# Kernel tuning notes

Measured on AMD Instinct MI355X. Metric: run time of the kernel, lower is better.

The kernel has to match this reference:

```python
import jax, jax.numpy as jnp
import numpy as np

WIN = (9, 9, 9)
EPS = 1e-05


def setup_inputs() -> dict:
    key = jax.random.key(0)
    k1, k2 = jax.random.split(key)
    shape = (2, 1, 160, 160, 160)  # [B, C=1, D, H, W]
    x = jax.random.normal(k1, shape, dtype=jnp.float32)
    y = jax.random.normal(k2, shape, dtype=jnp.float32)
    return {"x": x, "y": y}


def _convn(z, kernel):
    # dense 3D box-sum conv, VALID (inputs are pre-padded), NCDHW layout
    return jax.lax.conv_general_dilated(
        z, kernel, window_strides=(1, 1, 1), padding='VALID',
        dimension_numbers=('NCDHW', 'OIDHW', 'NCDHW'))


def reference(x, y):
    p = tuple(w // 2 for w in WIN)  # (4, 4, 4)
    pad_cfg = ((0, 0), (0, 0), (p[0], p[0]), (p[1], p[1]), (p[2], p[2]))
    kernel = jnp.ones((1, 1) + WIN, dtype=x.dtype)

    x_pad = jnp.pad(x, pad_cfg, mode='edge')      # replicate padding
    y_pad = jnp.pad(y, pad_cfg, mode='edge')
    ones_pad = jnp.pad(jnp.ones_like(x), pad_cfg, mode='edge')

    N = _convn(ones_pad, kernel)                  # local window counts (all = 729 here)
    xm = _convn(x_pad, kernel) / N                # local mean of x
    ym = _convn(y_pad, kernel) / N                # local mean of y
    x2 = _convn(x_pad * x_pad, kernel) / N        # local E[x^2]
    y2 = _convn(y_pad * y_pad, kernel) / N        # local E[y^2]
    xy = _convn(x_pad * y_pad, kernel) / N        # local E[xy]

    cross = xy - xm * ym
    var_x = x2 - xm * xm
    var_y = y2 - ym * ym
    ncc = cross * cross / (var_x * var_y + EPS)
    return -jnp.mean(ncc)
```

## Files before the change

### kernel.cpp

```cpp
#include <hip/hip_runtime.h>

#define DIM 160
#define SLICE (DIM * DIM)
#define TH 16
#define TW 16
#define CD 40

#define HIDX(c,i,j) ((c)*680 + (i)*28 + (j))
#define UIDX(c,i,j) ((c)*260 + (i)*16 + (j))

#define WSLIDE(dst, V0,V1,V2,V3,V4,V5,V6,V7,V8,V9,V10,V11) do {            \
    float s_ = (V0)+(V1)+(V2)+(V3)+(V4)+(V5)+(V6)+(V7)+(V8);               \
    float4 o_; o_.x = s_;                                                  \
    s_ += (V9)  - (V0); o_.y = s_;                                         \
    s_ += (V10) - (V1); o_.z = s_;                                         \
    s_ += (V11) - (V2); o_.w = s_;                                         \
    (dst) = o_; } while (0)

static __device__ __forceinline__ void barrier_novm()
{
    asm volatile("s_waitcnt lgkmcnt(0)" ::: "memory");
    __builtin_amdgcn_s_barrier();
    asm volatile("" ::: "memory");
}

__global__ __launch_bounds__(256, 2)
void lncc_kernel(const float* __restrict__ x, const float* __restrict__ y,
                 float* __restrict__ out)
{
    __shared__ __align__(16) float H[5 * 680];
    __shared__ __align__(16) float U[5 * 260];
    __shared__ float wsum[4];

    const int t  = threadIdx.x;
    const int w0 = blockIdx.x * TW;
    const int h0 = blockIdx.y * TH;
    const int bz = blockIdx.z;
    const int b   = bz >> 2;
    const int zo0 = (bz & 3) * CD;

    const float* xb = x + (size_t)b * (DIM * SLICE);
    const float* yb = y + (size_t)b * (DIM * SLICE);

    const int lt  = t - 160;
    const int lrw = lt >> 2;
    const int lq  = lt & 3;
    const int ghr = min(max(h0 - 4 + lrw, 0), DIM - 1);
    const int rowoff = ghr * DIM;
    const int gws = w0 + 4 * lq - 4;
    const bool ok0 = (gws >= 0);
    const bool ok2 = (gws + 8 <= DIM - 4);
    const int jj = 4 * lq;

    const int hcc = t >> 3;
    const int hq  = (t >> 1) & 3;
    const int hh  = t & 1;
    const int hr0 = hh * 8;
    const int hjj = 4 * hq;

    const int i4 = t >> 4;
    const int j4 = t & 15;

    float hist[9][5];
    float rs[5] = {0.f, 0.f, 0.f, 0.f, 0.f};
    float acc = 0.f;

    float4 lx0, lx1, lx2, ly0, ly1, ly2;

    auto issue_loads = [&](int zsl) {
        const float* xs = xb + (size_t)zsl * SLICE + rowoff;
        const float* ys = yb + (size_t)zsl * SLICE + rowoff;
        lx1 = *reinterpret_cast<const float4*>(xs + gws + 4);
        ly1 = *reinterpret_cast<const float4*>(ys + gws + 4);
        if (ok0) {
            lx0 = *reinterpret_cast<const float4*>(xs + gws);
            ly0 = *reinterpret_cast<const float4*>(ys + gws);
        } else {
            const float v = xs[0];       lx0 = make_float4(v, v, v, v);
            const float w = ys[0];       ly0 = make_float4(w, w, w, w);
        }
        if (ok2) {
            lx2 = *reinterpret_cast<const float4*>(xs + gws + 8);
            ly2 = *reinterpret_cast<const float4*>(ys + gws + 8);
        } else {
            const float v = xs[DIM - 1]; lx2 = make_float4(v, v, v, v);
            const float w = ys[DIM - 1]; ly2 = make_float4(w, w, w, w);
        }
    };

    const int zfirst = zo0 - 4;
    if (t >= 160) issue_loads(max(zfirst, 0));

    for (int base = 0; base < 54; base += 9) {
        #pragma unroll
        for (int p = 0; p < 9; ++p) {
            const int s = base + p;
            if (s <= 48) {
                if (s >= 1) {
                    const int cp = (p + 8) % 9;
                    float u[5];
                    #pragma unroll
                    for (int c = 0; c < 5; ++c) {
                        u[c] = U[UIDX(c, i4, j4)];
                        rs[c] += u[c];
                        hist[cp][c] = u[c];
                    }
                    if (s >= 9) {
                        const float inv = 1.0f / 729.0f;
                        const float xm = rs[0] * inv, ym = rs[1] * inv;
                        const float x2 = rs[2] * inv, y2 = rs[3] * inv;
                        const float xy = rs[4] * inv;
                        const float cross = xy - xm * ym;
                        const float vx = x2 - xm * xm;
                        const float vy = y2 - ym * ym;
                        acc += cross * cross / (vx * vy + 1e-5f);
                        const int po = (cp + 1) % 9;
                        #pragma unroll
                        for (int c = 0; c < 5; ++c)
                            rs[c] -= hist[po][c];
                    }
                }
                if (s <= 47 && t >= 160) {
                    float4 o;
                    WSLIDE(o, lx0.x,lx0.y,lx0.z,lx0.w, lx1.x,lx1.y,lx1.z,lx1.w,
                              lx2.x,lx2.y,lx2.z,lx2.w);
                    *reinterpret_cast<float4*>(&H[HIDX(0, lrw, jj)]) = o;
                    WSLIDE(o, ly0.x,ly0.y,ly0.z,ly0.w, ly1.x,ly1.y,ly1.z,ly1.w,
                              ly2.x,ly2.y,ly2.z,ly2.w);
                    *reinterpret_cast<float4*>(&H[HIDX(1, lrw, jj)]) = o;
                    float4 a0 = lx0 * lx0, a1 = lx1 * lx1, a2 = lx2 * lx2;
                    WSLIDE(o, a0.x,a0.y,a0.z,a0.w, a1.x,a1.y,a1.z,a1.w,
                              a2.x,a2.y,a2.z,a2.w);
                    *reinterpret_cast<float4*>(&H[HIDX(2, lrw, jj)]) = o;
                    a0 = ly0 * ly0; a1 = ly1 * ly1; a2 = ly2 * ly2;
                    WSLIDE(o, a0.x,a0.y,a0.z,a0.w, a1.x,a1.y,a1.z,a1.w,
                              a2.x,a2.y,a2.z,a2.w);
                    *reinterpret_cast<float4*>(&H[HIDX(3, lrw, jj)]) = o;
                    a0 = lx0 * ly0; a1 = lx1 * ly1; a2 = lx2 * ly2;
                    WSLIDE(o, a0.x,a0.y,a0.z,a0.w, a1.x,a1.y,a1.z,a1.w,
                              a2.x,a2.y,a2.z,a2.w);
                    *reinterpret_cast<float4*>(&H[HIDX(4, lrw, jj)]) = o;
                }
                barrier_novm();
                if (s <= 47 && t < 40) {
                    float4 sum = make_float4(0.f, 0.f, 0.f, 0.f);
                    #pragma unroll
                    for (int k = 0; k < 9; ++k)
                        sum += *reinterpret_cast<const float4*>(&H[HIDX(hcc, hr0 + k, hjj)]);
                    *reinterpret_cast<float4*>(&U[UIDX(hcc, hr0, hjj)]) = sum;
                    #pragma unroll
                    for (int m = 1; m < 8; ++m) {
                        sum += *reinterpret_cast<const float4*>(&H[HIDX(hcc, hr0 + m + 8, hjj)])
                             - *reinterpret_cast<const float4*>(&H[HIDX(hcc, hr0 + m - 1, hjj)]);
                        *reinterpret_cast<float4*>(&U[UIDX(hcc, hr0 + m, hjj)]) = sum;
                    }
                }
                if (s <= 46 && t >= 160)
                    issue_loads(min(max(zfirst + s + 1, 0), DIM - 1));
                barrier_novm();
            }
        }
    }

    __syncthreads();
    #pragma unroll
    for (int off = 32; off > 0; off >>= 1)
        acc += __shfl_down(acc, off, 64);
    const int wave = t >> 6;
    if ((t & 63) == 0) wsum[wave] = acc;
    __syncthreads();
    if (t == 0) {
        const float s = wsum[0] + wsum[1] + wsum[2] + wsum[3];
        atomicAdd(out, -s * (1.0f / 8192000.0f));
    }
}

extern "C" void kernel_launch(void* const* d_in, const int* in_sizes, int n_in,
                              void* d_out, int out_size, void* d_ws, size_t ws_size,
                              hipStream_t stream)
{
    const float* x = (const float*)d_in[0];
    const float* y = (const float*)d_in[1];
    float* out = (float*)d_out;

    hipMemsetAsync(out, 0, sizeof(float), stream);

    dim3 grid(DIM / TW, DIM / TH, 2 * (DIM / CD));
    lncc_kernel<<<grid, 256, 0, stream>>>(x, y, out);
}
```

Measured before the change: 165.2 us.

## Double-buffer slice loads and halve depth chunk for higher occupancy

Global loads for input slices are now alternately double-buffered into even and odd register sets, so each load is issued two slices ahead instead of one. This hides more memory latency behind the sliding-window work. The depth chunk per block drops from 40 to 20 slices, doubling the grid, and launch bounds request 4 blocks per CU instead of 2. In exchange, the 8-slice z halo is amortised over fewer outputs, so more redundant loads and window sums are done. The lower register budget may also cause spills.

```diff
diff --git a/kernel.cpp b/kernel.cpp
--- a/kernel.cpp
+++ b/kernel.cpp
@@ -4,7 +4,8 @@
 #define SLICE (DIM * DIM)
 #define TH 16
 #define TW 16
-#define CD 40
+#define CD 20
+#define NS (CD + 8)
 
 #define HIDX(c,i,j) ((c)*680 + (i)*28 + (j))
 #define UIDX(c,i,j) ((c)*260 + (i)*16 + (j))
@@ -24,7 +25,7 @@
     asm volatile("" ::: "memory");
 }
 
-__global__ __launch_bounds__(256, 2)
+__global__ __launch_bounds__(256, 4)
 void lncc_kernel(const float* __restrict__ x, const float* __restrict__ y,
                  float* __restrict__ out)
 {
@@ -36,8 +37,8 @@
     const int w0 = blockIdx.x * TW;
     const int h0 = blockIdx.y * TH;
     const int bz = blockIdx.z;
-    const int b   = bz >> 2;
-    const int zo0 = (bz & 3) * CD;
+    const int b   = bz >> 3;
+    const int zo0 = (bz & 7) * CD;
 
     const float* xb = x + (size_t)b * (DIM * SLICE);
     const float* yb = y + (size_t)b * (DIM * SLICE);
@@ -65,37 +66,61 @@
     float rs[5] = {0.f, 0.f, 0.f, 0.f, 0.f};
     float acc = 0.f;
 
-    float4 lx0, lx1, lx2, ly0, ly1, ly2;
-
-    auto issue_loads = [&](int zsl) {
+    float4 eX0, eX1, eX2, eY0, eY1, eY2;
+    float4 oX0, oX1, oX2, oY0, oY1, oY2;
+
+    auto issue_into = [&](int zsl, float4& X0, float4& X1, float4& X2,
+                                   float4& Y0, float4& Y1, float4& Y2) {
         const float* xs = xb + (size_t)zsl * SLICE + rowoff;
         const float* ys = yb + (size_t)zsl * SLICE + rowoff;
-        lx1 = *reinterpret_cast<const float4*>(xs + gws + 4);
-        ly1 = *reinterpret_cast<const float4*>(ys + gws + 4);
+        X1 = *reinterpret_cast<const float4*>(xs + gws + 4);
+        Y1 = *reinterpret_cast<const float4*>(ys + gws + 4);
         if (ok0) {
-            lx0 = *reinterpret_cast<const float4*>(xs + gws);
-            ly0 = *reinterpret_cast<const float4*>(ys + gws);
+            X0 = *reinterpret_cast<const float4*>(xs + gws);
+            Y0 = *reinterpret_cast<const float4*>(ys + gws);
         } else {
-            const float v = xs[0];       lx0 = make_float4(v, v, v, v);
-            const float w = ys[0];       ly0 = make_float4(w, w, w, w);
+            const float v = xs[0];       X0 = make_float4(v, v, v, v);
+            const float w = ys[0];       Y0 = make_float4(w, w, w, w);
         }
         if (ok2) {
-            lx2 = *reinterpret_cast<const float4*>(xs + gws + 8);
-            ly2 = *reinterpret_cast<const float4*>(ys + gws + 8);
+            X2 = *reinterpret_cast<const float4*>(xs + gws + 8);
+            Y2 = *reinterpret_cast<const float4*>(ys + gws + 8);
         } else {
-            const float v = xs[DIM - 1]; lx2 = make_float4(v, v, v, v);
-            const float w = ys[DIM - 1]; ly2 = make_float4(w, w, w, w);
+            const float v = xs[DIM - 1]; X2 = make_float4(v, v, v, v);
+            const float w = ys[DIM - 1]; Y2 = make_float4(w, w, w, w);
         }
     };
 
+    auto wsums_from = [&](const float4& X0, const float4& X1, const float4& X2,
+                          const float4& Y0, const float4& Y1, const float4& Y2) {
+        float4 o;
+        WSLIDE(o, X0.x,X0.y,X0.z,X0.w, X1.x,X1.y,X1.z,X1.w, X2.x,X2.y,X2.z,X2.w);
+        *reinterpret_cast<float4*>(&H[HIDX(0, lrw, jj)]) = o;
+        WSLIDE(o, Y0.x,Y0.y,Y0.z,Y0.w, Y1.x,Y1.y,Y1.z,Y1.w, Y2.x,Y2.y,Y2.z,Y2.w);
+        *reinterpret_cast<float4*>(&H[HIDX(1, lrw, jj)]) = o;
+        float4 a0 = X0 * X0, a1 = X1 * X1, a2 = X2 * X2;
+        WSLIDE(o, a0.x,a0.y,a0.z,a0.w, a1.x,a1.y,a1.z,a1.w, a2.x,a2.y,a2.z,a2.w);
+        *reinterpret_cast<float4*>(&H[HIDX(2, lrw, jj)]) = o;
+        a0 = Y0 * Y0; a1 = Y1 * Y1; a2 = Y2 * Y2;
+        WSLIDE(o, a0.x,a0.y,a0.z,a0.w, a1.x,a1.y,a1.z,a1.w, a2.x,a2.y,a2.z,a2.w);
+        *reinterpret_cast<float4*>(&H[HIDX(3, lrw, jj)]) = o;
+        a0 = X0 * Y0; a1 = X1 * Y1; a2 = X2 * Y2;
+        WSLIDE(o, a0.x,a0.y,a0.z,a0.w, a1.x,a1.y,a1.z,a1.w, a2.x,a2.y,a2.z,a2.w);
+        *reinterpret_cast<float4*>(&H[HIDX(4, lrw, jj)]) = o;
+    };
+
     const int zfirst = zo0 - 4;
-    if (t >= 160) issue_loads(max(zfirst, 0));
-
-    for (int base = 0; base < 54; base += 9) {
+    auto zclamp = [&](int s) { return min(max(zfirst + s, 0), DIM - 1); };
+    if (t >= 160) {
+        issue_into(zclamp(0), eX0, eX1, eX2, eY0, eY1, eY2);
+        issue_into(zclamp(1), oX0, oX1, oX2, oY0, oY1, oY2);
+    }
+
+    for (int base = 0; base < 36; base += 18) {
         #pragma unroll
-        for (int p = 0; p < 9; ++p) {
+        for (int p = 0; p < 18; ++p) {
             const int s = base + p;
-            if (s <= 48) {
+            if (s <= NS) {
                 if (s >= 1) {
                     const int cp = (p + 8) % 9;
                     float u[5];
@@ -120,29 +145,12 @@
                             rs[c] -= hist[po][c];
                     }
                 }
-                if (s <= 47 && t >= 160) {
-                    float4 o;
-                    WSLIDE(o, lx0.x,lx0.y,lx0.z,lx0.w, lx1.x,lx1.y,lx1.z,lx1.w,
-                              lx2.x,lx2.y,lx2.z,lx2.w);
-                    *reinterpret_cast<float4*>(&H[HIDX(0, lrw, jj)]) = o;
-                    WSLIDE(o, ly0.x,ly0.y,ly0.z,ly0.w, ly1.x,ly1.y,ly1.z,ly1.w,
-                              ly2.x,ly2.y,ly2.z,ly2.w);
-                    *reinterpret_cast<float4*>(&H[HIDX(1, lrw, jj)]) = o;
-                    float4 a0 = lx0 * lx0, a1 = lx1 * lx1, a2 = lx2 * lx2;
-                    WSLIDE(o, a0.x,a0.y,a0.z,a0.w, a1.x,a1.y,a1.z,a1.w,
-                              a2.x,a2.y,a2.z,a2.w);
-                    *reinterpret_cast<float4*>(&H[HIDX(2, lrw, jj)]) = o;
-                    a0 = ly0 * ly0; a1 = ly1 * ly1; a2 = ly2 * ly2;
-                    WSLIDE(o, a0.x,a0.y,a0.z,a0.w, a1.x,a1.y,a1.z,a1.w,
-                              a2.x,a2.y,a2.z,a2.w);
-                    *reinterpret_cast<float4*>(&H[HIDX(3, lrw, jj)]) = o;
-                    a0 = lx0 * ly0; a1 = lx1 * ly1; a2 = lx2 * ly2;
-                    WSLIDE(o, a0.x,a0.y,a0.z,a0.w, a1.x,a1.y,a1.z,a1.w,
-                              a2.x,a2.y,a2.z,a2.w);
-                    *reinterpret_cast<float4*>(&H[HIDX(4, lrw, jj)]) = o;
+                if (s <= NS - 1 && t >= 160) {
+                    if ((p & 1) == 0) wsums_from(eX0, eX1, eX2, eY0, eY1, eY2);
+                    else              wsums_from(oX0, oX1, oX2, oY0, oY1, oY2);
                 }
                 barrier_novm();
-                if (s <= 47 && t < 40) {
+                if (s <= NS - 1 && t < 40) {
                     float4 sum = make_float4(0.f, 0.f, 0.f, 0.f);
                     #pragma unroll
                     for (int k = 0; k < 9; ++k)
@@ -155,8 +163,10 @@
                         *reinterpret_cast<float4*>(&U[UIDX(hcc, hr0 + m, hjj)]) = sum;
                     }
                 }
-                if (s <= 46 && t >= 160)
-                    issue_loads(min(max(zfirst + s + 1, 0), DIM - 1));
+                if (s <= NS - 3 && t >= 160) {
+                    if ((p & 1) == 0) issue_into(zclamp(s + 2), eX0, eX1, eX2, eY0, eY1, eY2);
+                    else              issue_into(zclamp(s + 2), oX0, oX1, oX2, oY0, oY1, oY2);
+                }
                 barrier_novm();
             }
         }
```

New measurement: 363.2 us. +119.9%, slower.
